# Optimization experiments

Measured on AMD Instinct MI355X. Metric: run time of the kernel, lower is better.

The kernel has to match this reference:

```python
import jax, jax.numpy as jnp
import numpy as np

H = 256  # hidden_size
IN = 256  # input_size
OUT = 128  # output_size


def _gru_cell(x, h, Wx, bx, Wh, bh):
    # x: (B, in), h: (B, H); Wx: (3H, in), Wh: (3H, H)
    xt = x @ Wx.T + bx  # (B, 3H)
    ht = h @ Wh.T + bh  # (B, 3H)
    xr, xz, xn = jnp.split(xt, 3, axis=1)
    hr, hz, hn = jnp.split(ht, 3, axis=1)
    r = jax.nn.sigmoid(xr + hr)
    z = jax.nn.sigmoid(xz + hz)
    n = jnp.tanh(xn + r * hn)
    return z * h + (1.0 - z) * n


def setup_inputs() -> dict:
    key = jax.random.key(0)
    ks = jax.random.split(key, 12)
    std = 1.0 / np.sqrt(H)
    u = lambda k, shape: jax.random.uniform(k, shape, jnp.float32, -std, std)
    return {
        "x": jax.random.normal(ks[0], (128, 1024, IN), jnp.float32),
        "Wx0": u(ks[1], (3 * H, IN)), "bx0": u(ks[2], (3 * H,)),
        "Wh0": u(ks[3], (3 * H, H)), "bh0": u(ks[4], (3 * H,)),
        "Wx1": u(ks[5], (3 * H, H)), "bx1": u(ks[6], (3 * H,)),
        "Wh1": u(ks[7], (3 * H, H)), "bh1": u(ks[8], (3 * H,)),
        "Wo": u(ks[9], (OUT, H)), "bo": u(ks[10], (OUT,)),
    }


def reference(x, Wx0, bx0, Wh0, bh0, Wx1, bx1, Wh1, bh1, Wo, bo):
    B = x.shape[0]
    h_init = (jnp.zeros((B, H), x.dtype), jnp.zeros((B, H), x.dtype))

    def step(carry, x_t):
        h0, h1 = carry
        h0 = _gru_cell(x_t, h0, Wx0, bx0, Wh0, bh0)
        h1 = _gru_cell(h0, h1, Wx1, bx1, Wh1, bh1)
        return (h0, h1), None

    # scan over time: x transposed to (T, B, in)
    (h0, h1), _ = jax.lax.scan(step, h_init, jnp.swapaxes(x, 0, 1))
    return h1 @ Wo.T + bo
```

## Files before the change

### kernel.cpp

```cpp
#include <hip/hip_runtime.h>
#include <stdint.h>


#define NPAIR 64

#define XR0_OFF 0
#define XR1_OFF 262144
#define HR0_OFF 524288
#define CTR_OFF 655360
#define FLG_OFF 659456

#if defined(__has_builtin)
#if __has_builtin(__builtin_amdgcn_fdot2)
#define USE_DOT2 1
#endif
#if __has_builtin(__builtin_amdgcn_rcpf)
#define USE_RCP 1
#endif
#endif

typedef uint32_t u32x16 __attribute__((ext_vector_type(16)));
typedef _Float16 h2_t __attribute__((ext_vector_type(2)));
union H2U { uint32_t u; h2_t h; };
union FU  { uint32_t u; float f; };

__device__ __forceinline__ float bf2f(uint16_t b){ FU v; v.u=(uint32_t)b<<16; return v.f; }
__device__ __forceinline__ uint16_t f2bf(float f){
    FU v; v.f=f; uint32_t r=v.u+0x7fffu+((v.u>>16)&1u); return (uint16_t)(r>>16);
}
__device__ __forceinline__ float rcp_f(float x){
#ifdef USE_RCP
    return __builtin_amdgcn_rcpf(x);
#else
    return 1.0f/x;
#endif
}
__device__ __forceinline__ float sigmoid_f(float x){ return rcp_f(1.0f+__expf(-x)); }
__device__ __forceinline__ float tanh_f(float x){
    float ax=fabsf(x); float e=__expf(-2.0f*ax);
    float t=(1.0f-e)*rcp_f(1.0f+e); return x<0.0f?-t:t;
}
__device__ __forceinline__ float dot2acc(uint32_t w, uint32_t v, float acc){
#ifdef USE_DOT2
    H2U a,b; a.u=w; b.u=v;
    return __builtin_amdgcn_fdot2(a.h, b.h, acc, false);
#else
    FU x0,x1,y0,y1;
    x0.u=w<<16; x1.u=w&0xffff0000u; y0.u=v<<16; y1.u=v&0xffff0000u;
    acc=fmaf(x0.f,y0.f,acc); return fmaf(x1.f,y1.f,acc);
#endif
}
__device__ __forceinline__ uint32_t cvt_bfpair(uint32_t raw){
#ifdef USE_DOT2
    FU lo,hi; lo.u=raw<<16; hi.u=raw&0xffff0000u;
    H2U r; r.h[0]=(_Float16)lo.f; r.h[1]=(_Float16)hi.f; return r.u;
#else
    return raw;
#endif
}
__device__ __forceinline__ uint32_t packpair(float lo, float hi){
#ifdef USE_DOT2
    H2U r; r.h[0]=(_Float16)lo; r.h[1]=(_Float16)hi; return r.u;
#else
    return (uint32_t)f2bf(lo) | ((uint32_t)f2bf(hi)<<16);
#endif
}
__device__ __forceinline__ u32x16 load16_bf(const uint4* p){
    uint4 a=p[0], b=p[1], c=p[2], d=p[3];
    u32x16 v;
    v[0]=cvt_bfpair(a.x);  v[1]=cvt_bfpair(a.y);  v[2]=cvt_bfpair(a.z);  v[3]=cvt_bfpair(a.w);
    v[4]=cvt_bfpair(b.x);  v[5]=cvt_bfpair(b.y);  v[6]=cvt_bfpair(b.z);  v[7]=cvt_bfpair(b.w);
    v[8]=cvt_bfpair(c.x);  v[9]=cvt_bfpair(c.y);  v[10]=cvt_bfpair(c.z); v[11]=cvt_bfpair(c.w);
    v[12]=cvt_bfpair(d.x); v[13]=cvt_bfpair(d.y); v[14]=cvt_bfpair(d.z); v[15]=cvt_bfpair(d.w);
    return v;
}
__device__ __forceinline__ u32x16 load16_f32(const float2* p){
    u32x16 v;
#define LF(i) v[i] = packpair(p[i].x, p[i].y)
    LF(0);LF(1);LF(2);LF(3);LF(4);LF(5);LF(6);LF(7);
    LF(8);LF(9);LF(10);LF(11);LF(12);LF(13);LF(14);LF(15);
#undef LF
    return v;
}

#define RLX_LD(p)    __hip_atomic_load((p),        __ATOMIC_RELAXED, __HIP_MEMORY_SCOPE_AGENT)
#define RLX_ST(p,v)  __hip_atomic_store((p), (v),  __ATOMIC_RELAXED, __HIP_MEMORY_SCOPE_AGENT)
__device__ __forceinline__ uint64_t RLX_LD64(const uint64_t* p){
    return __hip_atomic_load(p, __ATOMIC_RELAXED, __HIP_MEMORY_SCOPE_AGENT);
}
__device__ __forceinline__ void RLX_ST64(uint64_t* p, uint64_t v){
    __hip_atomic_store(p, v, __ATOMIC_RELAXED, __HIP_MEMORY_SCOPE_AGENT);
}

#define BAR() do {                                              \
    asm volatile("s_waitcnt lgkmcnt(0)" ::: "memory");          \
    __builtin_amdgcn_s_barrier();                               \
    asm volatile("" ::: "memory");                              \
} while (0)

#define DOT16(WR, WZ, WN, G)                                                      \
    _Pragma("unroll")                                                             \
    for (int q = 0; q < 4; ++q) {                                                 \
        uint4 va = pa[4*(G)+q], vb = pb[4*(G)+q];                                 \
        ar0 = dot2acc(WR[4*q+0], va.x, ar0); ar1 = dot2acc(WR[4*q+0], vb.x, ar1); \
        az0 = dot2acc(WZ[4*q+0], va.x, az0); az1 = dot2acc(WZ[4*q+0], vb.x, az1); \
        an0 = dot2acc(WN[4*q+0], va.x, an0); an1 = dot2acc(WN[4*q+0], vb.x, an1); \
        ar0 = dot2acc(WR[4*q+1], va.y, ar0); ar1 = dot2acc(WR[4*q+1], vb.y, ar1); \
        az0 = dot2acc(WZ[4*q+1], va.y, az0); az1 = dot2acc(WZ[4*q+1], vb.y, az1); \
        an0 = dot2acc(WN[4*q+1], va.y, an0); an1 = dot2acc(WN[4*q+1], vb.y, an1); \
        ar0 = dot2acc(WR[4*q+2], va.z, ar0); ar1 = dot2acc(WR[4*q+2], vb.z, ar1); \
        az0 = dot2acc(WZ[4*q+2], va.z, az0); az1 = dot2acc(WZ[4*q+2], vb.z, az1); \
        an0 = dot2acc(WN[4*q+2], va.z, an0); an1 = dot2acc(WN[4*q+2], vb.z, an1); \
        ar0 = dot2acc(WR[4*q+3], va.w, ar0); ar1 = dot2acc(WR[4*q+3], vb.w, ar1); \
        az0 = dot2acc(WZ[4*q+3], va.w, az0); az1 = dot2acc(WZ[4*q+3], vb.w, az1); \
        an0 = dot2acc(WN[4*q+3], va.w, an0); an1 = dot2acc(WN[4*q+3], vb.w, an1); \
    }

__global__ void probe_init(const uint32_t* __restrict__ w,
                           uint32_t* __restrict__ ctr,
                           uint32_t* __restrict__ flag) {
    int i = threadIdx.x;
    for (int k = i; k < 4096; k += 1024) ctr[k] = 0u;
    if (i == 0) {
        int c = 0;
        for (int j = 0; j < 64; ++j) {
            uint32_t e = (w[j] >> 7) & 0xFFu;
            c += (e >= 0x60u && e <= 0x7Cu) ? 1 : 0;
        }
        flag[0] = (c >= 32) ? 1u : 0u;
    }
}

__global__ void __launch_bounds__(512) __attribute__((amdgpu_waves_per_eu(2, 2)))
gru10(const void* __restrict__ xin,
      const void* __restrict__ Wx0, const void* __restrict__ bx0,
      const void* __restrict__ Wh0, const void* __restrict__ bh0,
      const void* __restrict__ Wx1, const void* __restrict__ bx1,
      const void* __restrict__ Wh1, const void* __restrict__ bh1,
      const void* __restrict__ Wo,  const void* __restrict__ bo,
      void* __restrict__ out,
      uint32_t* __restrict__ ws)
{
    const int tid  = threadIdx.x;
    const int pair = blockIdx.x & (NPAIR - 1);
    const int role = blockIdx.x >> 6;
    const int p    = tid >> 1;
    const int hs   = tid & 1;

    uint64_t* XR0p = (uint64_t*)(ws + XR0_OFF) + pair * 2048;
    uint64_t* XR1p = (uint64_t*)(ws + XR1_OFF) + pair * 2048;
    uint64_t* HRp  = (uint64_t*)(ws + HR0_OFF) + pair * 1024;
    uint32_t* CTR  = ws + CTR_OFF;
    const int isbf = (int)ws[FLG_OFF];

    uint32_t* myprg   = CTR + role * 1024 + pair * 16;
    uint32_t* consprg = CTR + (role + 1) * 1024 + pair * 16;

    const void* Wsel; const void* bsel;
    if      (role == 0) { Wsel = Wx0; bsel = bx0; }
    else if (role == 1) { Wsel = Wh0; bsel = bh0; }
    else if (role == 2) { Wsel = Wx1; bsel = bx1; }
    else                { Wsel = Wh1; bsel = bh1; }

    u32x16 wr0,wr1,wr2,wr3, wz0,wz1,wz2,wz3, wn0,wn1,wn2,wn3;
    float br, bz, bn;
    if (isbf) {
        const uint4* W4 = (const uint4*)Wsel;
        const uint4* r0 = W4 + (size_t)p * 32 + hs * 16;
        const uint4* r1 = W4 + (size_t)(p + 256) * 32 + hs * 16;
        const uint4* r2 = W4 + (size_t)(p + 512) * 32 + hs * 16;
        wr0=load16_bf(r0);    wr1=load16_bf(r0+4);  wr2=load16_bf(r0+8);  wr3=load16_bf(r0+12);
        wz0=load16_bf(r1);    wz1=load16_bf(r1+4);  wz2=load16_bf(r1+8);  wz3=load16_bf(r1+12);
        wn0=load16_bf(r2);    wn1=load16_bf(r2+4);  wn2=load16_bf(r2+8);  wn3=load16_bf(r2+12);
        const uint16_t* bs = (const uint16_t*)bsel;
        br = bf2f(bs[p]); bz = bf2f(bs[p+256]); bn = bf2f(bs[p+512]);
    } else {
        const float2* W2 = (const float2*)Wsel;
        const float2* r0 = W2 + (size_t)p * 128 + hs * 64;
        const float2* r1 = W2 + (size_t)(p + 256) * 128 + hs * 64;
        const float2* r2 = W2 + (size_t)(p + 512) * 128 + hs * 64;
        wr0=load16_f32(r0);    wr1=load16_f32(r0+16); wr2=load16_f32(r0+32); wr3=load16_f32(r0+48);
        wz0=load16_f32(r1);    wz1=load16_f32(r1+16); wz2=load16_f32(r1+32); wz3=load16_f32(r1+48);
        wn0=load16_f32(r2);    wn1=load16_f32(r2+16); wn2=load16_f32(r2+32); wn3=load16_f32(r2+48);
        const float* bs = (const float*)bsel;
        br = bs[p]; bz = bs[p+256]; bn = bs[p+512];
    }

    __shared__ __align__(16) uint32_t sb[544];

    if (role == 0 || role == 2) {
        const uint32_t* xs32 = (const uint32_t*)xin;
        const float2*   xsf  = (const float2*)xin;
        const int bglob = pair * 2 + (tid >> 7);
        const int i128  = tid & 127;
        const int spos  = (tid >> 7) * 136 + i128 + ((i128 >> 6) << 2);
        uint32_t xpref = 0;
        uint2 pfh; pfh.x = 0; pfh.y = 0;
        if (role == 0 && tid < 256) {
            if (isbf) xpref = cvt_bfpair(xs32[(size_t)bglob * 131072 + i128]);
            else { float2 f = xsf[(size_t)bglob * 131072 + i128]; xpref = packpair(f.x, f.y); }
        }
        uint64_t* outring = (role == 0) ? XR0p : XR1p;
        uint32_t prog_seen = 0;

        for (int t = 0; t < 1024; ++t) {
            if (t >= 4 && prog_seen + 3 < (uint32_t)t) {
                do { prog_seen = RLX_LD(consprg);
                     if (prog_seen + 3 < (uint32_t)t) __builtin_amdgcn_s_sleep(2);
                } while (prog_seen + 3 < (uint32_t)t);
            }
            if (tid < 256) {
                uint32_t pk;
                if (role == 0) pk = xpref;
                else {
                    uint2 v = pfh;
                    const uint32_t want = (uint32_t)(t + 1);
                    if (v.y != want) {
                        const uint64_t* a = HRp + (t & 3) * 256 + tid;
                        uint64_t u;
                        do { u = RLX_LD64(a);
                             v.x = (uint32_t)u; v.y = (uint32_t)(u >> 32);
                             if (v.y != want) __builtin_amdgcn_s_sleep(1);
                        } while (v.y != want);
                    }
                    pk = v.x;
                }
                sb[(t & 1) * 272 + spos] = pk;
            }
            BAR();
            if (tid == 0 && !(t & 1)) RLX_ST(myprg, (uint32_t)t);
            if (tid < 256 && t < 1023) {
                if (role == 0) {
                    if (isbf) xpref = cvt_bfpair(xs32[(size_t)bglob * 131072 + (t+1)*128 + i128]);
                    else { float2 f = xsf[(size_t)bglob * 131072 + (t+1)*128 + i128]; xpref = packpair(f.x, f.y); }
                } else {
                    uint64_t u = RLX_LD64(HRp + ((t + 1) & 3) * 256 + tid);
                    pfh.x = (uint32_t)u; pfh.y = (uint32_t)(u >> 32);
                }
            }
            float ar0=0,ar1=0,az0=0,az1=0,an0=0,an1=0;
            {
                const uint4* pa = ((const uint4*)&sb[(t & 1) * 272]) + hs * 17;
                const uint4* pb = pa + 34;
                DOT16(wr0,wz0,wn0,0); DOT16(wr1,wz1,wn1,1);
                DOT16(wr2,wz2,wn2,2); DOT16(wr3,wz3,wn3,3);
            }
            float R0 = ar0 + __shfl_xor(ar0,1), R1 = ar1 + __shfl_xor(ar1,1);
            float Z0 = az0 + __shfl_xor(az0,1), Z1 = az1 + __shfl_xor(az1,1);
            float N0 = an0 + __shfl_xor(an0,1), N1 = an1 + __shfl_xor(an1,1);
            float sr = (hs ? R1 : R0) + br;
            float sz = (hs ? Z1 : Z0) + bz;
            float sn = (hs ? N1 : N0) + bn;
            H2U lo; lo.h[0] = (_Float16)sr; lo.h[1] = (_Float16)sz;
            H2U sn16; sn16.u = 0; sn16.h[0] = (_Float16)sn;
            uint32_t hi = (sn16.u & 0xFFFFu) | (((uint32_t)(t + 1)) << 16);
            RLX_ST64(outring + (t & 3) * 512 + 2 * p + hs,
                     (uint64_t)lo.u | ((uint64_t)hi << 32));
        }
    } else {
        const uint64_t* xr64 = (role == 1) ? XR0p : XR1p;
        float h_reg = 0.0f;
        for (int i = tid; i < 544; i += 512) sb[i] = 0u;
        uint2 pfx; pfx.x = 0; pfx.y = 0;
        uint32_t prog_seen = 0;
        const int hj   = p >> 1;
        const int hpos = hs * 136 + hj + ((hj >> 6) << 2);

        for (int t = 0; t < 1024; ++t) {
            if (role == 1 && t >= 4 && prog_seen + 3 < (uint32_t)t) {
                do { prog_seen = RLX_LD(consprg);
                     if (prog_seen + 3 < (uint32_t)t) __builtin_amdgcn_s_sleep(2);
                } while (prog_seen + 3 < (uint32_t)t);
            }
            uint2 v = pfx;
            const uint32_t want = (uint32_t)(t + 1);
            if ((v.y >> 16) != want) {
                const uint64_t* a = xr64 + (t & 3) * 512 + 2 * p + hs;
                uint64_t u;
                do { u = RLX_LD64(a);
                     v.x = (uint32_t)u; v.y = (uint32_t)(u >> 32);
                     if ((v.y >> 16) != want) __builtin_amdgcn_s_sleep(1);
                } while ((v.y >> 16) != want);
            }
            H2U ua; ua.u = v.x;
            H2U ub; ub.u = v.y & 0xFFFFu;
            float xr = (float)ua.h[0], xz = (float)ua.h[1], xn = (float)ub.h[0];
            BAR();
            if (tid == 0 && !(t & 1)) RLX_ST(myprg, (uint32_t)t);
            if (t < 1023) {
                uint64_t u = RLX_LD64(xr64 + ((t + 1) & 3) * 512 + 2 * p + hs);
                pfx.x = (uint32_t)u; pfx.y = (uint32_t)(u >> 32);
            }
            float ar0=0,ar1=0,az0=0,az1=0,an0=0,an1=0;
            {
                const uint4* pa = ((const uint4*)&sb[(t & 1) * 272]) + hs * 17;
                const uint4* pb = pa + 34;
                DOT16(wr0,wz0,wn0,0); DOT16(wr1,wz1,wn1,1);
                DOT16(wr2,wz2,wn2,2); DOT16(wr3,wz3,wn3,3);
            }
            float R0 = ar0 + __shfl_xor(ar0,1), R1 = ar1 + __shfl_xor(ar1,1);
            float Z0 = az0 + __shfl_xor(az0,1), Z1 = az1 + __shfl_xor(az1,1);
            float N0 = an0 + __shfl_xor(an0,1), N1 = an1 + __shfl_xor(an1,1);
            float r = sigmoid_f(xr + (hs ? R1 : R0) + br);
            float z = sigmoid_f(xz + (hs ? Z1 : Z0) + bz);
            float n = tanh_f(xn + r * ((hs ? N1 : N0) + bn));
            h_reg = z * h_reg + (1.0f - z) * n;
            float hp = __shfl_xor(h_reg, 2);
            if (!(tid & 2)) {
                uint32_t pk = packpair(h_reg, hp);
                sb[((t + 1) & 1) * 272 + hpos] = pk;
                if (role == 1)
                    RLX_ST64(HRp + (t & 3) * 256 + hs * 128 + hj,
                             (uint64_t)pk | ((uint64_t)(t + 1) << 32));
            }
        }
        BAR();
        if (tid == 0) RLX_ST(myprg, 1024u);

        if (role == 3 && tid < 256) {
            const int j = tid >> 1, bb = tid & 1;
            const uint32_t* hv = &sb[bb * 136];
            float acc;
            if (isbf) {
                acc = bf2f(((const uint16_t*)bo)[j]);
                const uint32_t* wo = (const uint32_t*)Wo + j * 128;
#pragma unroll 8
                for (int c = 0; c < 128; ++c)
                    acc = dot2acc(cvt_bfpair(wo[c]), hv[c + ((c >> 6) << 2)], acc);
                ((uint16_t*)out)[(pair * 2 + bb) * 128 + j] = f2bf(acc);
            } else {
                acc = ((const float*)bo)[j];
                const float2* wo = (const float2*)Wo + j * 128;
#pragma unroll 8
                for (int c = 0; c < 128; ++c) {
                    float2 f = wo[c];
                    acc = dot2acc(packpair(f.x, f.y), hv[c + ((c >> 6) << 2)], acc);
                }
                ((float*)out)[(pair * 2 + bb) * 128 + j] = acc;
            }
        }
    }
}

extern "C" void kernel_launch(void* const* d_in, const int* in_sizes, int n_in,
                              void* d_out, int out_size, void* d_ws, size_t ws_size,
                              hipStream_t stream) {
    uint32_t* ws  = (uint32_t*)d_ws;
    uint32_t* CTR = ws + CTR_OFF;
    uint32_t* FLG = ws + FLG_OFF;

    probe_init<<<dim3(1), dim3(1024), 0, stream>>>((const uint32_t*)d_in[1], CTR, FLG);
    gru10<<<dim3(256), dim3(512), 0, stream>>>(
        d_in[0], d_in[1], d_in[2], d_in[3], d_in[4],
        d_in[5], d_in[6], d_in[7], d_in[8], d_in[9], d_in[10],
        d_out, ws);
}
```

Before: 2.663 ms.

## Replace per-thread fdot2 GRU matvecs with MFMA 16x16x32 f16 tiles

Each role block now computes its 3H x 256 matvec for the batch pair with MFMA 16x16x32 f16 instructions instead of packed dot2 loops. Weights are held in registers as MFMA B fragments and hidden state is read from shared memory as A fragments. Bias is folded into the accumulator, and only the first lane quarter of each wave handles the ring stores and the gate math. The goal is to cut the VALU instruction count on the serial per-timestep critical path. In exchange, most MFMA output is wasted because only 2 of 16 batch rows are real, and elementwise and sync work is concentrated on fewer lanes.

```diff
diff --git a/kernel.cpp b/kernel.cpp
--- a/kernel.cpp
+++ b/kernel.cpp
@@ -19,8 +19,9 @@
 #endif
 #endif
 
-typedef uint32_t u32x16 __attribute__((ext_vector_type(16)));
-typedef _Float16 h2_t __attribute__((ext_vector_type(2)));
+typedef _Float16 half8 __attribute__((ext_vector_type(8)));
+typedef float    f32x4 __attribute__((ext_vector_type(4)));
+typedef _Float16 h2_t  __attribute__((ext_vector_type(2)));
 union H2U { uint32_t u; h2_t h; };
 union FU  { uint32_t u; float f; };
 
@@ -40,47 +41,24 @@
     float ax=fabsf(x); float e=__expf(-2.0f*ax);
     float t=(1.0f-e)*rcp_f(1.0f+e); return x<0.0f?-t:t;
 }
+__device__ __forceinline__ uint32_t bfpair_to_h2(uint32_t raw){
+    FU lo,hi; lo.u=raw<<16; hi.u=raw&0xffff0000u;
+    H2U r; r.h[0]=(_Float16)lo.f; r.h[1]=(_Float16)hi.f; return r.u;
+}
+__device__ __forceinline__ uint32_t f2_to_h2(float a, float b){
+    H2U r; r.h[0]=(_Float16)a; r.h[1]=(_Float16)b; return r.u;
+}
+__device__ __forceinline__ float hbits2f(uint32_t bits){
+    H2U t; t.u = bits & 0xffffu; return (float)t.h[0];
+}
 __device__ __forceinline__ float dot2acc(uint32_t w, uint32_t v, float acc){
 #ifdef USE_DOT2
     H2U a,b; a.u=w; b.u=v;
     return __builtin_amdgcn_fdot2(a.h, b.h, acc, false);
 #else
-    FU x0,x1,y0,y1;
-    x0.u=w<<16; x1.u=w&0xffff0000u; y0.u=v<<16; y1.u=v&0xffff0000u;
-    acc=fmaf(x0.f,y0.f,acc); return fmaf(x1.f,y1.f,acc);
-#endif
-}
-__device__ __forceinline__ uint32_t cvt_bfpair(uint32_t raw){
-#ifdef USE_DOT2
-    FU lo,hi; lo.u=raw<<16; hi.u=raw&0xffff0000u;
-    H2U r; r.h[0]=(_Float16)lo.f; r.h[1]=(_Float16)hi.f; return r.u;
-#else
-    return raw;
-#endif
-}
-__device__ __forceinline__ uint32_t packpair(float lo, float hi){
-#ifdef USE_DOT2
-    H2U r; r.h[0]=(_Float16)lo; r.h[1]=(_Float16)hi; return r.u;
-#else
-    return (uint32_t)f2bf(lo) | ((uint32_t)f2bf(hi)<<16);
-#endif
-}
-__device__ __forceinline__ u32x16 load16_bf(const uint4* p){
-    uint4 a=p[0], b=p[1], c=p[2], d=p[3];
-    u32x16 v;
-    v[0]=cvt_bfpair(a.x);  v[1]=cvt_bfpair(a.y);  v[2]=cvt_bfpair(a.z);  v[3]=cvt_bfpair(a.w);
-    v[4]=cvt_bfpair(b.x);  v[5]=cvt_bfpair(b.y);  v[6]=cvt_bfpair(b.z);  v[7]=cvt_bfpair(b.w);
-    v[8]=cvt_bfpair(c.x);  v[9]=cvt_bfpair(c.y);  v[10]=cvt_bfpair(c.z); v[11]=cvt_bfpair(c.w);
-    v[12]=cvt_bfpair(d.x); v[13]=cvt_bfpair(d.y); v[14]=cvt_bfpair(d.z); v[15]=cvt_bfpair(d.w);
-    return v;
-}
-__device__ __forceinline__ u32x16 load16_f32(const float2* p){
-    u32x16 v;
-#define LF(i) v[i] = packpair(p[i].x, p[i].y)
-    LF(0);LF(1);LF(2);LF(3);LF(4);LF(5);LF(6);LF(7);
-    LF(8);LF(9);LF(10);LF(11);LF(12);LF(13);LF(14);LF(15);
-#undef LF
-    return v;
+    H2U a,b; a.u=w; b.u=v;
+    return fmaf((float)a.h[1],(float)b.h[1], fmaf((float)a.h[0],(float)b.h[0],acc));
+#endif
 }
 
 #define RLX_LD(p)    __hip_atomic_load((p),        __ATOMIC_RELAXED, __HIP_MEMORY_SCOPE_AGENT)
@@ -98,23 +76,26 @@
     asm volatile("" ::: "memory");                              \
 } while (0)
 
-#define DOT16(WR, WZ, WN, G)                                                      \
-    _Pragma("unroll")                                                             \
-    for (int q = 0; q < 4; ++q) {                                                 \
-        uint4 va = pa[4*(G)+q], vb = pb[4*(G)+q];                                 \
-        ar0 = dot2acc(WR[4*q+0], va.x, ar0); ar1 = dot2acc(WR[4*q+0], vb.x, ar1); \
-        az0 = dot2acc(WZ[4*q+0], va.x, az0); az1 = dot2acc(WZ[4*q+0], vb.x, az1); \
-        an0 = dot2acc(WN[4*q+0], va.x, an0); an1 = dot2acc(WN[4*q+0], vb.x, an1); \
-        ar0 = dot2acc(WR[4*q+1], va.y, ar0); ar1 = dot2acc(WR[4*q+1], vb.y, ar1); \
-        az0 = dot2acc(WZ[4*q+1], va.y, az0); az1 = dot2acc(WZ[4*q+1], vb.y, az1); \
-        an0 = dot2acc(WN[4*q+1], va.y, an0); an1 = dot2acc(WN[4*q+1], vb.y, an1); \
-        ar0 = dot2acc(WR[4*q+2], va.z, ar0); ar1 = dot2acc(WR[4*q+2], vb.z, ar1); \
-        az0 = dot2acc(WZ[4*q+2], va.z, az0); az1 = dot2acc(WZ[4*q+2], vb.z, az1); \
-        an0 = dot2acc(WN[4*q+2], va.z, an0); an1 = dot2acc(WN[4*q+2], vb.z, an1); \
-        ar0 = dot2acc(WR[4*q+3], va.w, ar0); ar1 = dot2acc(WR[4*q+3], vb.w, ar1); \
-        az0 = dot2acc(WZ[4*q+3], va.w, az0); az1 = dot2acc(WZ[4*q+3], vb.w, az1); \
-        an0 = dot2acc(WN[4*q+3], va.w, an0); an1 = dot2acc(WN[4*q+3], vb.w, an1); \
+__device__ __forceinline__ f32x4 MFMA16(uint4 a, uint4 b, f32x4 c){
+    half8 A = __builtin_bit_cast(half8, a);
+    half8 B = __builtin_bit_cast(half8, b);
+    return __builtin_amdgcn_mfma_f32_16x16x32_f16(A, B, c, 0, 0, 0);
+}
+
+__device__ __forceinline__ uint4 ldfrag16(const void* W, int isbf, int row, int k0){
+    if (isbf){
+        uint4 raw = *(const uint4*)((const uint16_t*)W + (size_t)row*256 + k0);
+        raw.x = bfpair_to_h2(raw.x); raw.y = bfpair_to_h2(raw.y);
+        raw.z = bfpair_to_h2(raw.z); raw.w = bfpair_to_h2(raw.w);
+        return raw;
+    } else {
+        const float* p = (const float*)W + (size_t)row*256 + k0;
+        uint4 r;
+        r.x = f2_to_h2(p[0],p[1]); r.y = f2_to_h2(p[2],p[3]);
+        r.z = f2_to_h2(p[4],p[5]); r.w = f2_to_h2(p[6],p[7]);
+        return r;
     }
+}
 
 __global__ void probe_init(const uint32_t* __restrict__ w,
                            uint32_t* __restrict__ ctr,
@@ -132,7 +113,7 @@
 }
 
 __global__ void __launch_bounds__(512) __attribute__((amdgpu_waves_per_eu(2, 2)))
-gru10(const void* __restrict__ xin,
+gru11(const void* __restrict__ xin,
       const void* __restrict__ Wx0, const void* __restrict__ bx0,
       const void* __restrict__ Wh0, const void* __restrict__ bh0,
       const void* __restrict__ Wx1, const void* __restrict__ bx1,
@@ -144,8 +125,10 @@
     const int tid  = threadIdx.x;
     const int pair = blockIdx.x & (NPAIR - 1);
     const int role = blockIdx.x >> 6;
-    const int p    = tid >> 1;
-    const int hs   = tid & 1;
+    const int w    = tid >> 6;
+    const int l    = tid & 63;
+    const int lr   = l & 15;
+    const int lq   = l >> 4;
 
     uint64_t* XR0p = (uint64_t*)(ws + XR0_OFF) + pair * 2048;
     uint64_t* XR1p = (uint64_t*)(ws + XR1_OFF) + pair * 2048;
@@ -162,29 +145,19 @@
     else if (role == 2) { Wsel = Wx1; bsel = bx1; }
     else                { Wsel = Wh1; bsel = bh1; }
 
-    u32x16 wr0,wr1,wr2,wr3, wz0,wz1,wz2,wz3, wn0,wn1,wn2,wn3;
-    float br, bz, bn;
-    if (isbf) {
-        const uint4* W4 = (const uint4*)Wsel;
-        const uint4* r0 = W4 + (size_t)p * 32 + hs * 16;
-        const uint4* r1 = W4 + (size_t)(p + 256) * 32 + hs * 16;
-        const uint4* r2 = W4 + (size_t)(p + 512) * 32 + hs * 16;
-        wr0=load16_bf(r0);    wr1=load16_bf(r0+4);  wr2=load16_bf(r0+8);  wr3=load16_bf(r0+12);
-        wz0=load16_bf(r1);    wz1=load16_bf(r1+4);  wz2=load16_bf(r1+8);  wz3=load16_bf(r1+12);
-        wn0=load16_bf(r2);    wn1=load16_bf(r2+4);  wn2=load16_bf(r2+8);  wn3=load16_bf(r2+12);
-        const uint16_t* bs = (const uint16_t*)bsel;
-        br = bf2f(bs[p]); bz = bf2f(bs[p+256]); bn = bf2f(bs[p+512]);
-    } else {
-        const float2* W2 = (const float2*)Wsel;
-        const float2* r0 = W2 + (size_t)p * 128 + hs * 64;
-        const float2* r1 = W2 + (size_t)(p + 256) * 128 + hs * 64;
-        const float2* r2 = W2 + (size_t)(p + 512) * 128 + hs * 64;
-        wr0=load16_f32(r0);    wr1=load16_f32(r0+16); wr2=load16_f32(r0+32); wr3=load16_f32(r0+48);
-        wz0=load16_f32(r1);    wz1=load16_f32(r1+16); wz2=load16_f32(r1+32); wz3=load16_f32(r1+48);
-        wn0=load16_f32(r2);    wn1=load16_f32(r2+16); wn2=load16_f32(r2+32); wn3=load16_f32(r2+48);
-        const float* bs = (const float*)bsel;
-        br = bs[p]; bz = bs[p+256]; bn = bs[p+512];
-    }
+    uint4 bfr[6][8];
+    float bias[6];
+#pragma unroll
+    for (int g = 0; g < 3; ++g)
+#pragma unroll
+        for (int m = 0; m < 2; ++m) {
+            int row = g * 256 + 32 * w + 16 * m + lr;
+            bias[g*2+m] = isbf ? bf2f(((const uint16_t*)bsel)[row])
+                               : ((const float*)bsel)[row];
+#pragma unroll
+            for (int kk = 0; kk < 8; ++kk)
+                bfr[g*2+m][kk] = ldfrag16(Wsel, isbf, row, 32*kk + 8*lq);
+        }
 
     __shared__ __align__(16) uint32_t sb[544];
 
@@ -197,8 +170,8 @@
         uint32_t xpref = 0;
         uint2 pfh; pfh.x = 0; pfh.y = 0;
         if (role == 0 && tid < 256) {
-            if (isbf) xpref = cvt_bfpair(xs32[(size_t)bglob * 131072 + i128]);
-            else { float2 f = xsf[(size_t)bglob * 131072 + i128]; xpref = packpair(f.x, f.y); }
+            if (isbf) xpref = bfpair_to_h2(xs32[(size_t)bglob * 131072 + i128]);
+            else { float2 f = xsf[(size_t)bglob * 131072 + i128]; xpref = f2_to_h2(f.x, f.y); }
         }
         uint64_t* outring = (role == 0) ? XR0p : XR1p;
         uint32_t prog_seen = 0;
@@ -231,40 +204,53 @@
             if (tid == 0 && !(t & 1)) RLX_ST(myprg, (uint32_t)t);
             if (tid < 256 && t < 1023) {
                 if (role == 0) {
-                    if (isbf) xpref = cvt_bfpair(xs32[(size_t)bglob * 131072 + (t+1)*128 + i128]);
-                    else { float2 f = xsf[(size_t)bglob * 131072 + (t+1)*128 + i128]; xpref = packpair(f.x, f.y); }
+                    if (isbf) xpref = bfpair_to_h2(xs32[(size_t)bglob * 131072 + (t+1)*128 + i128]);
+                    else { float2 f = xsf[(size_t)bglob * 131072 + (t+1)*128 + i128]; xpref = f2_to_h2(f.x, f.y); }
                 } else {
                     uint64_t u = RLX_LD64(HRp + ((t + 1) & 3) * 256 + tid);
                     pfh.x = (uint32_t)u; pfh.y = (uint32_t)(u >> 32);
                 }
             }
-            float ar0=0,ar1=0,az0=0,az1=0,an0=0,an1=0;
-            {
-                const uint4* pa = ((const uint4*)&sb[(t & 1) * 272]) + hs * 17;
-                const uint4* pb = pa + 34;
-                DOT16(wr0,wz0,wn0,0); DOT16(wr1,wz1,wn1,1);
-                DOT16(wr2,wz2,wn2,2); DOT16(wr3,wz3,wn3,3);
-            }
-            float R0 = ar0 + __shfl_xor(ar0,1), R1 = ar1 + __shfl_xor(ar1,1);
-            float Z0 = az0 + __shfl_xor(az0,1), Z1 = az1 + __shfl_xor(az1,1);
-            float N0 = an0 + __shfl_xor(an0,1), N1 = an1 + __shfl_xor(an1,1);
-            float sr = (hs ? R1 : R0) + br;
-            float sz = (hs ? Z1 : Z0) + bz;
-            float sn = (hs ? N1 : N0) + bn;
-            H2U lo; lo.h[0] = (_Float16)sr; lo.h[1] = (_Float16)sz;
-            H2U sn16; sn16.u = 0; sn16.h[0] = (_Float16)sn;
-            uint32_t hi = (sn16.u & 0xFFFFu) | (((uint32_t)(t + 1)) << 16);
-            RLX_ST64(outring + (t & 3) * 512 + 2 * p + hs,
-                     (uint64_t)lo.u | ((uint64_t)hi << 32));
-        }
+            const uint32_t* abase = &sb[(t & 1) * 272 + (lr & 1) * 136];
+            uint4 afr[8];
+#pragma unroll
+            for (int kk = 0; kk < 8; ++kk) {
+                int j0 = 16*kk + 4*lq;
+                afr[kk] = *(const uint4*)&abase[j0 + ((j0 >> 6) << 2)];
+            }
+            f32x4 acc[6];
+#pragma unroll
+            for (int i6 = 0; i6 < 6; ++i6)
+                acc[i6] = (f32x4){bias[i6], bias[i6], bias[i6], bias[i6]};
+#pragma unroll
+            for (int kk = 0; kk < 8; ++kk)
+#pragma unroll
+                for (int i6 = 0; i6 < 6; ++i6)
+                    acc[i6] = MFMA16(afr[kk], bfr[i6][kk], acc[i6]);
+            if (lq == 0) {
+                const uint32_t want = (uint32_t)(t + 1);
+#pragma unroll
+                for (int m = 0; m < 2; ++m) {
+                    int u = 32 * w + 16 * m + lr;
+#pragma unroll
+                    for (int b = 0; b < 2; ++b) {
+                        H2U lo; lo.h[0] = (_Float16)acc[m][b]; lo.h[1] = (_Float16)acc[2+m][b];
+                        H2U hn; hn.u = 0; hn.h[0] = (_Float16)acc[4+m][b];
+                        uint32_t hi = (hn.u & 0xFFFFu) | (want << 16);
+                        RLX_ST64(outring + (t & 3) * 512 + 2 * u + b,
+                                 (uint64_t)lo.u | ((uint64_t)hi << 32));
+                    }
+                }
+            }
+        }
+        BAR();
+        if (tid == 0) RLX_ST(myprg, 1024u);
     } else {
         const uint64_t* xr64 = (role == 1) ? XR0p : XR1p;
-        float h_reg = 0.0f;
         for (int i = tid; i < 544; i += 512) sb[i] = 0u;
-        uint2 pfx; pfx.x = 0; pfx.y = 0;
+        float hreg[2][2] = {{0.f,0.f},{0.f,0.f}};
+        uint64_t cur[4]; cur[0]=cur[1]=cur[2]=cur[3]=0;
         uint32_t prog_seen = 0;
-        const int hj   = p >> 1;
-        const int hpos = hs * 136 + hj + ((hj >> 6) << 2);
 
         for (int t = 0; t < 1024; ++t) {
             if (role == 1 && t >= 4 && prog_seen + 3 < (uint32_t)t) {
@@ -272,46 +258,86 @@
                      if (prog_seen + 3 < (uint32_t)t) __builtin_amdgcn_s_sleep(2);
                 } while (prog_seen + 3 < (uint32_t)t);
             }
-            uint2 v = pfx;
             const uint32_t want = (uint32_t)(t + 1);
-            if ((v.y >> 16) != want) {
-                const uint64_t* a = xr64 + (t & 3) * 512 + 2 * p + hs;
-                uint64_t u;
-                do { u = RLX_LD64(a);
-                     v.x = (uint32_t)u; v.y = (uint32_t)(u >> 32);
-                     if ((v.y >> 16) != want) __builtin_amdgcn_s_sleep(1);
-                } while ((v.y >> 16) != want);
-            }
-            H2U ua; ua.u = v.x;
-            H2U ub; ub.u = v.y & 0xFFFFu;
-            float xr = (float)ua.h[0], xz = (float)ua.h[1], xn = (float)ub.h[0];
+            if (lq == 0) {
+#pragma unroll
+                for (int m = 0; m < 2; ++m)
+#pragma unroll
+                    for (int b = 0; b < 2; ++b) {
+                        int e = m * 2 + b;
+                        int u = 32 * w + 16 * m + lr;
+                        if ((uint32_t)(cur[e] >> 48) != want) {
+                            const uint64_t* a = xr64 + (t & 3) * 512 + 2 * u + b;
+                            uint64_t uu;
+                            do { uu = RLX_LD64(a);
+                                 if ((uint32_t)(uu >> 48) != want) __builtin_amdgcn_s_sleep(1);
+                            } while ((uint32_t)(uu >> 48) != want);
+                            cur[e] = uu;
+                        }
+                    }
+            }
             BAR();
             if (tid == 0 && !(t & 1)) RLX_ST(myprg, (uint32_t)t);
-            if (t < 1023) {
-                uint64_t u = RLX_LD64(xr64 + ((t + 1) & 3) * 512 + 2 * p + hs);
-                pfx.x = (uint32_t)u; pfx.y = (uint32_t)(u >> 32);
-            }
-            float ar0=0,ar1=0,az0=0,az1=0,an0=0,an1=0;
-            {
-                const uint4* pa = ((const uint4*)&sb[(t & 1) * 272]) + hs * 17;
-                const uint4* pb = pa + 34;
-                DOT16(wr0,wz0,wn0,0); DOT16(wr1,wz1,wn1,1);
-                DOT16(wr2,wz2,wn2,2); DOT16(wr3,wz3,wn3,3);
-            }
-            float R0 = ar0 + __shfl_xor(ar0,1), R1 = ar1 + __shfl_xor(ar1,1);
-            float Z0 = az0 + __shfl_xor(az0,1), Z1 = az1 + __shfl_xor(az1,1);
-            float N0 = an0 + __shfl_xor(an0,1), N1 = an1 + __shfl_xor(an1,1);
-            float r = sigmoid_f(xr + (hs ? R1 : R0) + br);
-            float z = sigmoid_f(xz + (hs ? Z1 : Z0) + bz);
-            float n = tanh_f(xn + r * ((hs ? N1 : N0) + bn));
-            h_reg = z * h_reg + (1.0f - z) * n;
-            float hp = __shfl_xor(h_reg, 2);
-            if (!(tid & 2)) {
-                uint32_t pk = packpair(h_reg, hp);
-                sb[((t + 1) & 1) * 272 + hpos] = pk;
-                if (role == 1)
-                    RLX_ST64(HRp + (t & 3) * 256 + hs * 128 + hj,
-                             (uint64_t)pk | ((uint64_t)(t + 1) << 32));
+            float srv[4], szv[4], snv[4];
+            if (lq == 0) {
+#pragma unroll
+                for (int e = 0; e < 4; ++e) {
+                    uint32_t loq = (uint32_t)cur[e];
+                    srv[e] = hbits2f(loq);
+                    szv[e] = hbits2f(loq >> 16);
+                    snv[e] = hbits2f((uint32_t)(cur[e] >> 32));
+                }
+                if (t < 1023) {
+#pragma unroll
+                    for (int m = 0; m < 2; ++m)
+#pragma unroll
+                        for (int b = 0; b < 2; ++b) {
+                            int u = 32 * w + 16 * m + lr;
+                            cur[m*2+b] = RLX_LD64(xr64 + ((t + 1) & 3) * 512 + 2 * u + b);
+                        }
+                }
+            }
+            const uint32_t* abase = &sb[(t & 1) * 272 + (lr & 1) * 136];
+            uint4 afr[8];
+#pragma unroll
+            for (int kk = 0; kk < 8; ++kk) {
+                int j0 = 16*kk + 4*lq;
+                afr[kk] = *(const uint4*)&abase[j0 + ((j0 >> 6) << 2)];
+            }
+            f32x4 acc[6];
+#pragma unroll
+            for (int i6 = 0; i6 < 6; ++i6)
+                acc[i6] = (f32x4){bias[i6], bias[i6], bias[i6], bias[i6]};
+#pragma unroll
+            for (int kk = 0; kk < 8; ++kk)
+#pragma unroll
+                for (int i6 = 0; i6 < 6; ++i6)
+                    acc[i6] = MFMA16(afr[kk], bfr[i6][kk], acc[i6]);
+            if (lq == 0) {
+#pragma unroll
+                for (int m = 0; m < 2; ++m)
+#pragma unroll
+                    for (int b = 0; b < 2; ++b) {
+                        int e = m * 2 + b;
+                        float r = sigmoid_f(srv[e] + acc[m][b]);
+                        float z = sigmoid_f(szv[e] + acc[2+m][b]);
+                        float n = tanh_f  (snv[e] + r * acc[4+m][b]);
+                        hreg[m][b] = z * hreg[m][b] + (1.0f - z) * n;
+                    }
+#pragma unroll
+                for (int m = 0; m < 2; ++m)
+#pragma unroll
+                    for (int b = 0; b < 2; ++b) {
+                        float hp = __shfl_xor(hreg[m][b], 1);
+                        if (!(l & 1)) {
+                            uint32_t pk = f2_to_h2(hreg[m][b], hp);
+                            int j = 16 * w + 8 * m + (lr >> 1);
+                            sb[((t + 1) & 1) * 272 + b * 136 + j + ((j >> 6) << 2)] = pk;
+                            if (role == 1)
+                                RLX_ST64(HRp + (t & 3) * 256 + b * 128 + j,
+                                         (uint64_t)pk | ((uint64_t)want << 32));
+                        }
+                    }
             }
         }
         BAR();
@@ -326,7 +352,7 @@
                 const uint32_t* wo = (const uint32_t*)Wo + j * 128;
 #pragma unroll 8
                 for (int c = 0; c < 128; ++c)
-                    acc = dot2acc(cvt_bfpair(wo[c]), hv[c + ((c >> 6) << 2)], acc);
+                    acc = dot2acc(bfpair_to_h2(wo[c]), hv[c + ((c >> 6) << 2)], acc);
                 ((uint16_t*)out)[(pair * 2 + bb) * 128 + j] = f2bf(acc);
             } else {
                 acc = ((const float*)bo)[j];
@@ -334,7 +360,7 @@
 #pragma unroll 8
                 for (int c = 0; c < 128; ++c) {
                     float2 f = wo[c];
-                    acc = dot2acc(packpair(f.x, f.y), hv[c + ((c >> 6) << 2)], acc);
+                    acc = dot2acc(f2_to_h2(f.x, f.y), hv[c + ((c >> 6) << 2)], acc);
                 }
                 ((float*)out)[(pair * 2 + bb) * 128 + j] = acc;
             }
@@ -350,7 +376,7 @@
     uint32_t* FLG = ws + FLG_OFF;
 
     probe_init<<<dim3(1), dim3(1024), 0, stream>>>((const uint32_t*)d_in[1], CTR, FLG);
-    gru10<<<dim3(256), dim3(512), 0, stream>>>(
+    gru11<<<dim3(256), dim3(512), 0, stream>>>(
         d_in[0], d_in[1], d_in[2], d_in[3], d_in[4],
         d_in[5], d_in[6], d_in[7], d_in[8], d_in[9], d_in[10],
         d_out, ws);
```

New measurement: 3.942 ms. +48.1%, slower.
